# Kernel optimization log

Hardware: AMD Instinct MI355X
Metric: run time of the kernel (lower is better)

## Reference

```python
import jax, jax.numpy as jnp
import numpy as np

H = 4            # attention heads (HGTConv and SGFormer)
HID = 128        # hidden_dim
D = HID // H     # per-head dim in HGT
OUT = 128        # out_dim
L = 2            # number of HGT layers
NE, NA = 60000, 30000
E_EE, E_EA, E_AE = 150000, 75000, 75000


def setup_inputs() -> dict:
    ks = iter(jax.random.split(jax.random.key(0), 64))

    def nrm(shape, s=0.05):
        return jax.random.normal(next(ks), shape, dtype=jnp.float32) * s

    return {
        "x_entity": nrm((NE, HID), 1.0),
        "x_attr": nrm((NA, HID), 1.0),
        "Wkqv_ent": nrm((L, HID, 3 * HID)), "bkqv_ent": jnp.zeros((L, 3 * HID), jnp.float32),
        "Wkqv_att": nrm((L, HID, 3 * HID)), "bkqv_att": jnp.zeros((L, 3 * HID), jnp.float32),
        "Wout_ent": nrm((L, HID, HID)), "bout_ent": jnp.zeros((L, HID), jnp.float32),
        "Wout_att": nrm((L, HID, HID)), "bout_att": jnp.zeros((L, HID), jnp.float32),
        "skip_ent": jnp.ones((L,), jnp.float32), "skip_att": jnp.ones((L,), jnp.float32),
        "a_rel": nrm((L, 3, H, D, D), 0.1), "m_rel": nrm((L, 3, H, D, D), 0.1),
        "p_rel": jnp.ones((L, 3, H), jnp.float32),
        "ln_ent_g": jnp.ones((HID,), jnp.float32), "ln_ent_b": jnp.zeros((HID,), jnp.float32),
        "sg_fc_W": nrm((HID, HID)), "sg_fc_b": jnp.zeros((HID,), jnp.float32),
        "sg_ln0_g": jnp.ones((HID,), jnp.float32), "sg_ln0_b": jnp.zeros((HID,), jnp.float32),
        "sg_Wq": nrm((HID, HID * H)), "sg_bq": jnp.zeros((HID * H,), jnp.float32),
        "sg_Wk": nrm((HID, HID * H)), "sg_bk": jnp.zeros((HID * H,), jnp.float32),
        "sg_Wv": nrm((HID, HID * H)), "sg_bv": jnp.zeros((HID * H,), jnp.float32),
        "sg_ln1_g": jnp.ones((HID,), jnp.float32), "sg_ln1_b": jnp.zeros((HID,), jnp.float32),
        "proj_W1": nrm((HID, OUT)), "proj_b1": jnp.zeros((OUT,), jnp.float32),
        "proj_W2": nrm((OUT, OUT)), "proj_b2": jnp.zeros((OUT,), jnp.float32),
        "ei_ee": jax.random.randint(next(ks), (2, E_EE), 0, NE),
        "ei_ea": jnp.stack([jax.random.randint(next(ks), (E_EA,), 0, NE),
                            jax.random.randint(next(ks), (E_EA,), 0, NA)]),
        "ei_ae": jnp.stack([jax.random.randint(next(ks), (E_AE,), 0, NA),
                            jax.random.randint(next(ks), (E_AE,), 0, NE)]),
    }


def _ln(x, g, b, eps=1e-5):
    mu = x.mean(-1, keepdims=True)
    var = ((x - mu) ** 2).mean(-1, keepdims=True)
    return (x - mu) * jax.lax.rsqrt(var + eps) * g + b


def _seg_softmax(alpha, idx, n):
    # numerically stable softmax over edges grouped by destination node
    m = jax.ops.segment_max(alpha, idx, num_segments=n)
    e = jnp.exp(alpha - m[idx])
    s = jax.ops.segment_sum(e, idx, num_segments=n)
    return e / (s[idx] + 1e-16)


def _hgt_layer(x_e, x_a, Wkqv_e, bkqv_e, Wkqv_a, bkqv_a, Wout_e, bout_e,
               Wout_a, bout_a, sk_e, sk_a, a_rel, m_rel, p_rel,
               ei_ee, ei_ea, ei_ae):
    ne, na = x_e.shape[0], x_a.shape[0]
    # HeteroDictLinear producing [k|q|v], split along channels then reshape [N,H,D]
    kqv_e = (x_e @ Wkqv_e + bkqv_e).reshape(ne, 3, H, D)
    kqv_a = (x_a @ Wkqv_a + bkqv_a).reshape(na, 3, H, D)
    kd = {"e": kqv_e[:, 0], "a": kqv_a[:, 0]}
    qd = {"e": kqv_e[:, 1], "a": kqv_a[:, 1]}
    vd = {"e": kqv_e[:, 2], "a": kqv_a[:, 2]}
    nd = {"e": ne, "a": na}
    scale = 1.0 / float(np.sqrt(D))
    buf = {"e": [], "a": []}
    for t, (src, dst, ei) in enumerate([("e", "e", ei_ee), ("e", "a", ei_ea), ("a", "e", ei_ae)]):
        kt = jnp.einsum('nhd,hde->nhe', kd[src], a_rel[t])  # per-relation key transform (k_rel)
        vt = jnp.einsum('nhd,hde->nhe', vd[src], m_rel[t])  # per-relation value transform (v_rel)
        al = (qd[dst][ei[1]] * kt[ei[0]]).sum(-1) * p_rel[t] * scale  # [E,H]
        buf[dst].append((al, vt[ei[0]], ei[1]))
    outs = {}
    for dst in ("e", "a"):
        # joint softmax over ALL incoming edge types of this node type
        al = jnp.concatenate([b[0] for b in buf[dst]], 0)
        ve = jnp.concatenate([b[1] for b in buf[dst]], 0)
        ix = jnp.concatenate([b[2] for b in buf[dst]], 0)
        w = _seg_softmax(al, ix, nd[dst])
        outs[dst] = jax.ops.segment_sum(ve * w[..., None], ix,
                                        num_segments=nd[dst]).reshape(nd[dst], HID)
    o_e = jax.nn.gelu(outs["e"], approximate=False) @ Wout_e + bout_e
    o_a = jax.nn.gelu(outs["a"], approximate=False) @ Wout_a + bout_a
    g_e, g_a = jax.nn.sigmoid(sk_e), jax.nn.sigmoid(sk_a)
    return g_e * o_e + (1.0 - g_e) * x_e, g_a * o_a + (1.0 - g_a) * x_a


def reference(x_entity, x_attr, Wkqv_ent, bkqv_ent, Wkqv_att, bkqv_att,
              Wout_ent, bout_ent, Wout_att, bout_att, skip_ent, skip_att,
              a_rel, m_rel, p_rel, ln_ent_g, ln_ent_b,
              sg_fc_W, sg_fc_b, sg_ln0_g, sg_ln0_b, sg_Wq, sg_bq, sg_Wk, sg_bk,
              sg_Wv, sg_bv, sg_ln1_g, sg_ln1_b,
              proj_W1, proj_b1, proj_W2, proj_b2, ei_ee, ei_ea, ei_ae):
    h_e, h_a = x_entity, x_attr
    for l in range(L):
        h_e, h_a = _hgt_layer(h_e, h_a, Wkqv_ent[l], bkqv_ent[l], Wkqv_att[l], bkqv_att[l],
                              Wout_ent[l], bout_ent[l], Wout_att[l], bout_att[l],
                              skip_ent[l], skip_att[l], a_rel[l], m_rel[l], p_rel[l],
                              ei_ee, ei_ea, ei_ae)
        h_e = jax.nn.gelu(h_e, approximate=False)
        h_a = jax.nn.gelu(h_a, approximate=False)
    # SGFormer trans_conv: fc -> LN -> ReLU -> linear global attention -> residual -> LN
    n = h_e.shape[0]
    z0 = jax.nn.relu(_ln(h_e @ sg_fc_W + sg_fc_b, sg_ln0_g, sg_ln0_b))
    q = (z0 @ sg_Wq + sg_bq).reshape(n, H, HID)
    k = (z0 @ sg_Wk + sg_bk).reshape(n, H, HID)
    v = (z0 @ sg_Wv + sg_bv).reshape(n, H, HID)
    qs = q / jnp.linalg.norm(q)  # global Frobenius norm, as in SGFormer
    kn = k / jnp.linalg.norm(k)
    kvs = jnp.einsum('lhm,lhd->hmd', kn, v)
    num = jnp.einsum('nhm,hmd->nhd', qs, kvs) + float(n) * v
    den = jnp.einsum('nhm,hm->nh', qs, kn.sum(0))[..., None] + float(n)
    attn = (num / den).mean(1)  # mean over heads -> [n, HID]
    h_global = _ln(0.5 * attn + 0.5 * z0, sg_ln1_g, sg_ln1_b)  # residual alpha=0.5
    # alpha-blend (self.alpha = 0.1) + entity LayerNorm + projector MLP
    h_ent = _ln(0.9 * h_e + 0.1 * h_global, ln_ent_g, ln_ent_b)
    return jax.nn.relu(h_ent @ proj_W1 + proj_b1) @ proj_W2 + proj_b2
```

## Files before the change

kernel.cpp:

```cpp
#include <hip/hip_runtime.h>

#define NE 60000
#define NA 30000
#define E_EE 150000
#define E_EA 75000
#define E_AE 75000
#define SCALE 0.17677669529663689f

__device__ __forceinline__ float bf2f(unsigned short u) {
  return __uint_as_float(((unsigned)u) << 16);
}
__device__ __forceinline__ unsigned short f2bf(float f) {
  unsigned u = __float_as_uint(f);
  u = u + 0x7FFFu + ((u >> 16) & 1u);
  return (unsigned short)(u >> 16);
}
__device__ __forceinline__ float ldc(const float* p) { return *p; }
__device__ __forceinline__ float ldc(const unsigned short* p) { return bf2f(*p); }
__device__ __forceinline__ float gelu_f(float x) {
  return 0.5f * x * (1.0f + erff(x * 0.7071067811865476f));
}

__global__ __launch_bounds__(256) void wrel_k(
    const float* __restrict__ Wk_e, const float* __restrict__ Wk_a,
    const float* __restrict__ bk_e, const float* __restrict__ bk_a,
    const float* __restrict__ a_rel, const float* __restrict__ m_rel,
    float* __restrict__ Wkt, float* __restrict__ Wvt,
    float* __restrict__ bkt, float* __restrict__ bvt) {
  int t = blockIdx.x;
  int part = blockIdx.y;
  const float* W = (t < 2) ? Wk_e : Wk_a;
  const float* bb = (t < 2) ? bk_e : bk_a;
  const float* A = (part ? m_rel : a_rel) + t * 4096;
  int coff = part ? 256 : 0;
  float* Wo = (part ? Wvt : Wkt) + t * 16384;
  float* bo = (part ? bvt : bkt) + t * 128;
  __shared__ float As[4096];
  for (int u = threadIdx.x; u < 4096; u += 256) As[u] = A[u];
  __syncthreads();
  for (int u = threadIdx.x; u < 16384; u += 256) {
    int i = u >> 7, c = u & 127;
    int hh = c >> 5, e = c & 31;
    const float* wr = W + i * 384 + coff + hh * 32;
    const float* ar = As + hh * 1024 + e;
    float acc = 0.f;
#pragma unroll
    for (int d = 0; d < 32; ++d) acc = fmaf(wr[d], ar[d * 32], acc);
    Wo[u] = acc;
  }
  if (threadIdx.x < 128) {
    int c = threadIdx.x, hh = c >> 5, e = c & 31;
    const float* br = bb + coff + hh * 32;
    const float* ar = As + hh * 1024 + e;
    float acc = 0.f;
#pragma unroll
    for (int d = 0; d < 32; ++d) acc = fmaf(br[d], ar[d * 32], acc);
    bo[c] = acc;
  }
}

template <int ACT, int EPI>
__global__ __launch_bounds__(256) void gemm128_k(
    const float* __restrict__ X, int ldx,
    const float* __restrict__ W, int ldw,
    const float* __restrict__ bias, int N,
    float* __restrict__ fout, unsigned short* __restrict__ bout, int ldo,
    const float* __restrict__ skipp, float* __restrict__ ssq) {
  __shared__ float Xs[128 * 32];
  __shared__ float Ws[32 * 128];
  const int tid = threadIdx.x;
  const int ti = tid >> 4;
  const int tj = tid & 15;
  const int row0 = blockIdx.x * 128;
  const int cb = blockIdx.y * 128;
  const int c0 = cb + tj * 4;
  const int c1 = cb + 64 + tj * 4;

  float acc[8][8];
  {
    float bc[8] = {0.f, 0.f, 0.f, 0.f, 0.f, 0.f, 0.f, 0.f};
    if (bias) {
#pragma unroll
      for (int j = 0; j < 4; ++j) { bc[j] = bias[c0 + j]; bc[4 + j] = bias[c1 + j]; }
    }
#pragma unroll
    for (int i = 0; i < 8; ++i)
#pragma unroll
      for (int j = 0; j < 8; ++j) acc[i][j] = bc[j];
  }

  for (int ks = 0; ks < 128; ks += 32) {
    __syncthreads();
    for (int v = tid; v < 1024; v += 256) {
      int kq = v & 7, r = v >> 3;
      int rg = row0 + r; if (rg >= N) rg = N - 1;
      float4 x4 = *reinterpret_cast<const float4*>(X + (size_t)rg * ldx + ks + kq * 4);
      if (ACT == 1) {
        x4.x = gelu_f(x4.x); x4.y = gelu_f(x4.y);
        x4.z = gelu_f(x4.z); x4.w = gelu_f(x4.w);
      }
      *reinterpret_cast<float4*>(&Xs[r * 32 + ((kq ^ ((r >> 3) & 7)) << 2)]) = x4;
    }
    for (int v = tid; v < 1024; v += 256) {
      int cq = v & 31, k = v >> 5;
      *reinterpret_cast<float4*>(&Ws[k * 128 + cq * 4]) =
          *reinterpret_cast<const float4*>(W + (size_t)(ks + k) * ldw + cb + cq * 4);
    }
    __syncthreads();
#pragma unroll
    for (int k = 0; k < 32; k += 4) {
      float xr[8][4];
#pragma unroll
      for (int i = 0; i < 8; ++i)
        *reinterpret_cast<float4*>(xr[i]) = *reinterpret_cast<const float4*>(
            &Xs[(ti * 8 + i) * 32 + ((((k >> 2)) ^ (ti & 7)) << 2)]);
      float wr[4][8];
#pragma unroll
      for (int dk = 0; dk < 4; ++dk) {
        *reinterpret_cast<float4*>(&wr[dk][0]) =
            *reinterpret_cast<const float4*>(&Ws[(k + dk) * 128 + tj * 4]);
        *reinterpret_cast<float4*>(&wr[dk][4]) =
            *reinterpret_cast<const float4*>(&Ws[(k + dk) * 128 + 64 + tj * 4]);
      }
#pragma unroll
      for (int i = 0; i < 8; ++i)
#pragma unroll
        for (int dk = 0; dk < 4; ++dk)
#pragma unroll
          for (int j = 0; j < 8; ++j)
            acc[i][j] = fmaf(xr[i][dk], wr[dk][j], acc[i][j]);
    }
  }

  if (EPI == 0 || EPI == 1) {
#pragma unroll
    for (int i = 0; i < 8; ++i) {
      int rg = row0 + ti * 8 + i;
      if (rg < N) {
        float4 a = make_float4(acc[i][0], acc[i][1], acc[i][2], acc[i][3]);
        float4 b = make_float4(acc[i][4], acc[i][5], acc[i][6], acc[i][7]);
        if (EPI == 1) {
          a.x = fmaxf(a.x, 0.f); a.y = fmaxf(a.y, 0.f);
          a.z = fmaxf(a.z, 0.f); a.w = fmaxf(a.w, 0.f);
          b.x = fmaxf(b.x, 0.f); b.y = fmaxf(b.y, 0.f);
          b.z = fmaxf(b.z, 0.f); b.w = fmaxf(b.w, 0.f);
        }
        *reinterpret_cast<float4*>(fout + (size_t)rg * ldo + c0) = a;
        *reinterpret_cast<float4*>(fout + (size_t)rg * ldo + c1) = b;
      }
    }
  } else if (EPI == 2) {
    float loc = 0.f;
#pragma unroll
    for (int i = 0; i < 8; ++i) {
      int rg = row0 + ti * 8 + i;
      if (rg < N) {
        ushort4 s0, s1;
        s0.x = f2bf(acc[i][0]); s0.y = f2bf(acc[i][1]);
        s0.z = f2bf(acc[i][2]); s0.w = f2bf(acc[i][3]);
        s1.x = f2bf(acc[i][4]); s1.y = f2bf(acc[i][5]);
        s1.z = f2bf(acc[i][6]); s1.w = f2bf(acc[i][7]);
        *reinterpret_cast<ushort4*>(bout + (size_t)rg * ldo + c0) = s0;
        *reinterpret_cast<ushort4*>(bout + (size_t)rg * ldo + c1) = s1;
#pragma unroll
        for (int j = 0; j < 8; ++j) loc += acc[i][j] * acc[i][j];
      }
    }
    if (ssq) {
      __syncthreads();
      Xs[tid] = loc;
      __syncthreads();
      if (tid < 128) Xs[tid] += Xs[tid + 128];
      __syncthreads();
      if (tid < 64) {
        float v = Xs[tid] + Xs[tid + 64];
#pragma unroll
        for (int m = 32; m > 0; m >>= 1) v += __shfl_down(v, m, 64);
        if (tid == 0) atomicAdd(ssq, v);
      }
    }
  } else {
    float g = 1.f / (1.f + expf(-*skipp));
    float g1 = 1.f - g;
#pragma unroll
    for (int i = 0; i < 8; ++i) {
      int rg = row0 + ti * 8 + i;
      if (rg < N) {
        float4 o0 = *reinterpret_cast<const float4*>(fout + (size_t)rg * ldo + c0);
        float4 o1 = *reinterpret_cast<const float4*>(fout + (size_t)rg * ldo + c1);
        float4 a, b;
        a.x = gelu_f(g * acc[i][0] + g1 * o0.x);
        a.y = gelu_f(g * acc[i][1] + g1 * o0.y);
        a.z = gelu_f(g * acc[i][2] + g1 * o0.z);
        a.w = gelu_f(g * acc[i][3] + g1 * o0.w);
        b.x = gelu_f(g * acc[i][4] + g1 * o1.x);
        b.y = gelu_f(g * acc[i][5] + g1 * o1.y);
        b.z = gelu_f(g * acc[i][6] + g1 * o1.z);
        b.w = gelu_f(g * acc[i][7] + g1 * o1.w);
        *reinterpret_cast<float4*>(fout + (size_t)rg * ldo + c0) = a;
        *reinterpret_cast<float4*>(fout + (size_t)rg * ldo + c1) = b;
      }
    }
  }
}

__global__ __launch_bounds__(256) void deg_k(const int* __restrict__ ei, int E,
                                             int* __restrict__ deg) {
  int i = blockIdx.x * 256 + threadIdx.x;
  if (i < E) atomicAdd(&deg[ei[E + i]], 1);
}

__global__ __launch_bounds__(1024) void scan_k(int* __restrict__ deg_cursor,
                                               int* __restrict__ rowptr, int n) {
  __shared__ int sd[1024];
  __shared__ int carry;
  int tid = threadIdx.x;
  if (tid == 0) carry = 0;
  __syncthreads();
  for (int base = 0; base < n; base += 1024) {
    int v = (base + tid < n) ? deg_cursor[base + tid] : 0;
    sd[tid] = v;
    __syncthreads();
    for (int off = 1; off < 1024; off <<= 1) {
      int t = (tid >= off) ? sd[tid - off] : 0;
      __syncthreads();
      sd[tid] += t;
      __syncthreads();
    }
    int c0 = carry;
    if (base + tid < n) {
      int excl = c0 + sd[tid] - v;
      rowptr[base + tid] = excl;
      deg_cursor[base + tid] = excl;
    }
    __syncthreads();
    if (tid == 0) carry = c0 + sd[1023];
    __syncthreads();
  }
  if (tid == 0) rowptr[n] = carry;
}

__global__ __launch_bounds__(256) void fill_k(const int* __restrict__ ei, int E,
                                              int* __restrict__ cursor,
                                              int* __restrict__ entries,
                                              int srcoff, int tag) {
  int i = blockIdx.x * 256 + threadIdx.x;
  if (i < E) {
    int pos = atomicAdd(&cursor[ei[E + i]], 1);
    entries[pos] = (ei[i] + srcoff) | (tag << 30);
  }
}

__global__ __launch_bounds__(256) void hgt_gather_k(
    const float* __restrict__ q, const unsigned short* __restrict__ ktbl,
    const unsigned short* __restrict__ vtbl, const int* __restrict__ rowptr,
    const int* __restrict__ entries, const float* __restrict__ pbase, int nd,
    float* __restrict__ out) {
  int g = blockIdx.x * 8 + (threadIdx.x >> 5);
  int dst = g >> 2, h = g & 3, c = threadIdx.x & 31;
  if (dst >= nd) return;
  int col = h * 32 + c;
  float qv = q[(size_t)dst * 128 + col];
  int i0 = rowptr[dst], i1 = rowptr[dst + 1];
  float sum = 0.f, acc = 0.f;
  for (int i = i0; i < i1; ++i) {
    int e = entries[i];
    int lin = e & 0x3FFFFFFF;
    int tag = (unsigned)e >> 30;
    float part = qv * bf2f(ktbl[(size_t)lin * 128 + col]);
#pragma unroll
    for (int m = 16; m > 0; m >>= 1) part += __shfl_xor(part, m);
    float w = expf(part * SCALE * pbase[tag * 8 + h]);
    sum += w;
    acc = fmaf(w, bf2f(vtbl[(size_t)lin * 128 + col]), acc);
  }
  out[(size_t)dst * 128 + col] = acc / (sum + 1e-16f);
}

template <typename AT, typename BT>
__global__ __launch_bounds__(128) void ln_k(const AT* __restrict__ A,
                                            const BT* __restrict__ B, float alpha,
                                            float beta, const float* __restrict__ g,
                                            const float* __restrict__ b,
                                            float* __restrict__ out, int relu) {
  int row = blockIdx.x;
  int t = threadIdx.x;
  float v = alpha * ldc(A + (size_t)row * 128 + t);
  if (B) v += beta * ldc(B + (size_t)row * 128 + t);
  float s1 = v, s2 = v * v;
#pragma unroll
  for (int m = 32; m > 0; m >>= 1) {
    s1 += __shfl_xor(s1, m, 64);
    s2 += __shfl_xor(s2, m, 64);
  }
  __shared__ float r1[2], r2[2];
  int w = t >> 6;
  if ((t & 63) == 0) { r1[w] = s1; r2[w] = s2; }
  __syncthreads();
  float S1 = r1[0] + r1[1], S2 = r2[0] + r2[1];
  float mu = S1 * (1.f / 128.f);
  float var = S2 * (1.f / 128.f) - mu * mu;
  float rr = rsqrtf(fmaxf(var, 0.f) + 1e-5f);
  float o = (v - mu) * rr * g[t] + b[t];
  if (relu) o = fmaxf(o, 0.f);
  out[(size_t)row * 128 + t] = o;
}

__global__ __launch_bounds__(256) void kvsred_k(const unsigned short* __restrict__ Kb,
                                                const unsigned short* __restrict__ Vb,
                                                float* __restrict__ part,
                                                float* __restrict__ ksum, int chunk) {
  const int h = blockIdx.y;
  const int n0 = blockIdx.x * chunk;
  const int iters = chunk >> 3;
  __shared__ float ks[8][132];
  __shared__ float vs[8][132];
  const int tid = threadIdx.x;
  const int ti = tid >> 4, tj = tid & 15;

  const int sw = tid >> 7;
  const int sni = (tid >> 4) & 7;
  const int sc = (tid & 15) << 3;
  const unsigned short* src =
      (sw ? Vb : Kb) + (size_t)(n0 + sni) * 512 + h * 128 + sc;
  float* dstrow = (sw ? &vs[0][0] : &ks[0][0]) + sni * 132 + sc;

  float acc[8][8];
#pragma unroll
  for (int i = 0; i < 8; ++i)
#pragma unroll
    for (int j = 0; j < 8; ++j) acc[i][j] = 0.f;
  float ksloc = 0.f;

  uint4 r = *reinterpret_cast<const uint4*>(src);
  for (int it = 0; it < iters; ++it) {
    __syncthreads();
    float4 lo, hi;
    lo.x = bf2f((unsigned short)(r.x & 0xffffu)); lo.y = bf2f((unsigned short)(r.x >> 16));
    lo.z = bf2f((unsigned short)(r.y & 0xffffu)); lo.w = bf2f((unsigned short)(r.y >> 16));
    hi.x = bf2f((unsigned short)(r.z & 0xffffu)); hi.y = bf2f((unsigned short)(r.z >> 16));
    hi.z = bf2f((unsigned short)(r.w & 0xffffu)); hi.w = bf2f((unsigned short)(r.w >> 16));
    *reinterpret_cast<float4*>(dstrow) = lo;
    *reinterpret_cast<float4*>(dstrow + 4) = hi;
    if (it + 1 < iters)
      r = *reinterpret_cast<const uint4*>(src + (size_t)(it + 1) * 8 * 512);
    __syncthreads();
#pragma unroll
    for (int ni = 0; ni < 8; ++ni) {
      float kk[8], vv[8];
      *reinterpret_cast<float4*>(kk) =
          *reinterpret_cast<const float4*>(&ks[ni][ti * 4]);
      *reinterpret_cast<float4*>(kk + 4) =
          *reinterpret_cast<const float4*>(&ks[ni][64 + ti * 4]);
      *reinterpret_cast<float4*>(vv) =
          *reinterpret_cast<const float4*>(&vs[ni][tj * 4]);
      *reinterpret_cast<float4*>(vv + 4) =
          *reinterpret_cast<const float4*>(&vs[ni][64 + tj * 4]);
#pragma unroll
      for (int i = 0; i < 8; ++i)
#pragma unroll
        for (int j = 0; j < 8; ++j) acc[i][j] = fmaf(kk[i], vv[j], acc[i][j]);
      if (tid < 128) ksloc += ks[ni][tid];
    }
  }
  float* pb = part + (size_t)(blockIdx.x * 4 + h) * 16384;
#pragma unroll
  for (int i = 0; i < 8; ++i) {
    int m = ti * 4 + (i & 3) + ((i >> 2) << 6);
    *reinterpret_cast<float4*>(pb + m * 128 + tj * 4) =
        make_float4(acc[i][0], acc[i][1], acc[i][2], acc[i][3]);
    *reinterpret_cast<float4*>(pb + m * 128 + 64 + tj * 4) =
        make_float4(acc[i][4], acc[i][5], acc[i][6], acc[i][7]);
  }
  if (tid < 128) atomicAdd(&ksum[h * 128 + tid], ksloc);
}

__global__ __launch_bounds__(256) void kvsfin_k(const float* __restrict__ part,
                                                float* __restrict__ kvs, int G) {
  int c = blockIdx.x * 256 + threadIdx.x;
  int hh = c >> 14, md = c & 16383;
  const float* p = part + (size_t)hh * 16384 + md;
  float s = 0.f;
#pragma unroll 4
  for (int g = 0; g < G; ++g) s += p[(size_t)g * 65536];
  kvs[c] = s;
}

__global__ __launch_bounds__(256) void sgapply_k(const unsigned short* __restrict__ Qb,
                                                 const unsigned short* __restrict__ Vb,
                                                 const float* __restrict__ kvs,
                                                 const float* __restrict__ ksum,
                                                 const float* __restrict__ ssqq,
                                                 const float* __restrict__ ssqk,
                                                 unsigned short* __restrict__ attnb) {
  __shared__ float Qs[32 * 132];
  __shared__ float Ws[64 * 128];
  __shared__ float dred[32][9];
  __shared__ float den_s[32];
  __shared__ float fsh;
  const int tid = threadIdx.x;
  const int ct = tid & 31, rt = tid >> 5;
  const int row0 = blockIdx.x * 32;
  if (tid == 0) fsh = 1.0f / (sqrtf(*ssqq) * sqrtf(*ssqk));
  float out[4][4];
#pragma unroll
  for (int i = 0; i < 4; ++i)
#pragma unroll
    for (int j = 0; j < 4; ++j) out[i][j] = 0.f;

  for (int h = 0; h < 4; ++h) {
    __syncthreads();
    for (int u = tid; u < 1024; u += 256) {
      int r = u >> 5, c = (u & 31) << 2;
      ushort4 q4 = *reinterpret_cast<const ushort4*>(
          Qb + (size_t)(row0 + r) * 512 + h * 128 + c);
      float4 v = make_float4(bf2f(q4.x), bf2f(q4.y), bf2f(q4.z), bf2f(q4.w));
      *reinterpret_cast<float4*>(&Qs[r * 132 + c]) = v;
    }
    __syncthreads();
    {
      int r = tid >> 3, seg = tid & 7;
      const float* kp = ksum + h * 128 + seg * 16;
      const float* qp = Qs + r * 132 + seg * 16;
      float p = 0.f;
#pragma unroll
      for (int c = 0; c < 16; ++c) p = fmaf(qp[c], kp[c], p);
      dred[r][seg] = p;
    }
    __syncthreads();
    if (tid < 32) {
      float t = 0.f;
#pragma unroll
      for (int s8 = 0; s8 < 8; ++s8) t += dred[tid][s8];
      den_s[tid] = t * fsh + 60000.0f;
    }
    float acc[4][4];
#pragma unroll
    for (int i = 0; i < 4; ++i)
#pragma unroll
      for (int j = 0; j < 4; ++j) acc[i][j] = 0.f;
    for (int kk = 0; kk < 2; ++kk) {
      __syncthreads();
      for (int u = tid; u < 2048; u += 256) {
        int r = u >> 5, c = (u & 31) << 2;
        *reinterpret_cast<float4*>(&Ws[r * 128 + c]) =
            *reinterpret_cast<const float4*>(kvs + (size_t)h * 16384 +
                                             (size_t)(kk * 64 + r) * 128 + c);
      }
      __syncthreads();
#pragma unroll 4
      for (int k = 0; k < 64; k += 4) {
        float w[4][4];
#pragma unroll
        for (int dk = 0; dk < 4; ++dk)
          *reinterpret_cast<float4*>(w[dk]) =
              *reinterpret_cast<const float4*>(&Ws[(k + dk) * 128 + (ct << 2)]);
#pragma unroll
        for (int i = 0; i < 4; ++i) {
          float xv[4];
          *reinterpret_cast<float4*>(xv) =
              *reinterpret_cast<const float4*>(&Qs[(rt * 4 + i) * 132 + kk * 64 + k]);
#pragma unroll
          for (int dk = 0; dk < 4; ++dk)
#pragma unroll
            for (int j = 0; j < 4; ++j) acc[i][j] = fmaf(xv[dk], w[dk][j], acc[i][j]);
        }
      }
    }
    float f = fsh;
#pragma unroll
    for (int i = 0; i < 4; ++i) {
      int rg = row0 + rt * 4 + i;
      ushort4 v4 = *reinterpret_cast<const ushort4*>(
          Vb + (size_t)rg * 512 + h * 128 + (ct << 2));
      float rd = 1.0f / den_s[rt * 4 + i];
      out[i][0] += (acc[i][0] * f + 60000.0f * bf2f(v4.x)) * rd;
      out[i][1] += (acc[i][1] * f + 60000.0f * bf2f(v4.y)) * rd;
      out[i][2] += (acc[i][2] * f + 60000.0f * bf2f(v4.z)) * rd;
      out[i][3] += (acc[i][3] * f + 60000.0f * bf2f(v4.w)) * rd;
    }
  }
#pragma unroll
  for (int i = 0; i < 4; ++i) {
    int rg = row0 + rt * 4 + i;
    ushort4 s4;
    s4.x = f2bf(0.25f * out[i][0]); s4.y = f2bf(0.25f * out[i][1]);
    s4.z = f2bf(0.25f * out[i][2]); s4.w = f2bf(0.25f * out[i][3]);
    *reinterpret_cast<ushort4*>(attnb + (size_t)rg * 128 + (ct << 2)) = s4;
  }
}

extern "C" void kernel_launch(void* const* d_in, const int* in_sizes, int n_in,
                              void* d_out, int out_size, void* d_ws, size_t ws_size,
                              hipStream_t stream) {
  const float* x_ent = (const float*)d_in[0];
  const float* x_att = (const float*)d_in[1];
  const float* Wkqv_e = (const float*)d_in[2];
  const float* bkqv_e = (const float*)d_in[3];
  const float* Wkqv_a = (const float*)d_in[4];
  const float* bkqv_a = (const float*)d_in[5];
  const float* Wout_e = (const float*)d_in[6];
  const float* bout_e = (const float*)d_in[7];
  const float* Wout_a = (const float*)d_in[8];
  const float* bout_a = (const float*)d_in[9];
  const float* skip_e = (const float*)d_in[10];
  const float* skip_a = (const float*)d_in[11];
  const float* a_rel = (const float*)d_in[12];
  const float* m_rel = (const float*)d_in[13];
  const float* p_rel = (const float*)d_in[14];
  const float* ln_ent_g = (const float*)d_in[15];
  const float* ln_ent_b = (const float*)d_in[16];
  const float* sg_fc_W = (const float*)d_in[17];
  const float* sg_fc_b = (const float*)d_in[18];
  const float* sg_ln0_g = (const float*)d_in[19];
  const float* sg_ln0_b = (const float*)d_in[20];
  const float* sg_Wq = (const float*)d_in[21];
  const float* sg_bq = (const float*)d_in[22];
  const float* sg_Wk = (const float*)d_in[23];
  const float* sg_bk = (const float*)d_in[24];
  const float* sg_Wv = (const float*)d_in[25];
  const float* sg_bv = (const float*)d_in[26];
  const float* sg_ln1_g = (const float*)d_in[27];
  const float* sg_ln1_b = (const float*)d_in[28];
  const float* proj_W1 = (const float*)d_in[29];
  const float* proj_b1 = (const float*)d_in[30];
  const float* proj_W2 = (const float*)d_in[31];
  const float* proj_b2 = (const float*)d_in[32];
  const int* ei_ee = (const int*)d_in[33];
  const int* ei_ea = (const int*)d_in[34];
  const int* ei_ae = (const int*)d_in[35];

  char* ws = (char*)d_ws;
  const size_t O_HE = 0;
  const size_t O_HA = 30720000;
  const size_t O_Z0 = 46080000;
  const size_t O_WKT = 76800000;
  const size_t O_WVT = 76996608;
  const size_t O_BKT = 77193216;
  const size_t O_BVT = 77194752;
  const size_t O_KVS = 77196288;
  const size_t O_RPE = 77460544;
  const size_t O_RPA = O_RPE + 240064;
  const size_t O_CUE = O_RPA + 120064;
  const size_t O_CUA = O_CUE + 240000;
  const size_t O_ENE = O_CUA + 120000;
  const size_t O_ENA = O_ENE + 900000;
  const size_t O_UN = O_ENA + 300000;
  float* q_e = (float*)(ws + O_UN);
  float* q_a = (float*)(ws + O_UN + 30720000);
  unsigned short* ktbl = (unsigned short*)(ws + O_UN + 46080000);
  unsigned short* vtbl = (unsigned short*)(ws + O_UN + 84480000);
  float* tmpf = (float*)(ws + O_UN);
  unsigned short* Vb = (unsigned short*)(ws + O_UN);
  unsigned short* KQb = (unsigned short*)(ws + O_UN + 61440000);
  unsigned short* attnb = (unsigned short*)(ws + O_HA);

  float* h_e = (float*)(ws + O_HE);
  float* h_a = (float*)(ws + O_HA);
  float* z0 = (float*)(ws + O_Z0);
  float* Wkt = (float*)(ws + O_WKT);
  float* Wvt = (float*)(ws + O_WVT);
  float* bkt = (float*)(ws + O_BKT);
  float* bvt = (float*)(ws + O_BVT);
  float* kvs = (float*)(ws + O_KVS);
  float* ksum = (float*)(ws + O_KVS + 262144);
  float* ssq_q = (float*)(ws + O_KVS + 262144 + 2048);
  float* ssq_k = ssq_q + 1;
  int* rowptr_e = (int*)(ws + O_RPE);
  int* rowptr_a = (int*)(ws + O_RPA);
  int* cursor_e = (int*)(ws + O_CUE);
  int* cursor_a = (int*)(ws + O_CUA);
  int* entries_e = (int*)(ws + O_ENE);
  int* entries_a = (int*)(ws + O_ENA);

  const int GB_E = (NE + 127) / 128;
  const int GB_A = (NA + 127) / 128;

  hipMemcpyAsync(h_e, x_ent, (size_t)NE * 128 * 4, hipMemcpyDeviceToDevice, stream);
  hipMemcpyAsync(h_a, x_att, (size_t)NA * 128 * 4, hipMemcpyDeviceToDevice, stream);

  hipMemsetAsync(ws + O_CUE, 0, 360000, stream);
  deg_k<<<(E_EE + 255) / 256, 256, 0, stream>>>(ei_ee, E_EE, cursor_e);
  deg_k<<<(E_AE + 255) / 256, 256, 0, stream>>>(ei_ae, E_AE, cursor_e);
  deg_k<<<(E_EA + 255) / 256, 256, 0, stream>>>(ei_ea, E_EA, cursor_a);
  scan_k<<<1, 1024, 0, stream>>>(cursor_e, rowptr_e, NE);
  scan_k<<<1, 1024, 0, stream>>>(cursor_a, rowptr_a, NA);
  fill_k<<<(E_EE + 255) / 256, 256, 0, stream>>>(ei_ee, E_EE, cursor_e, entries_e, 0, 0);
  fill_k<<<(E_AE + 255) / 256, 256, 0, stream>>>(ei_ae, E_AE, cursor_e, entries_e, NE, 1);
  fill_k<<<(E_EA + 255) / 256, 256, 0, stream>>>(ei_ea, E_EA, cursor_a, entries_a, 0, 0);

  for (int l = 0; l < 2; ++l) {
    const float* Wke = Wkqv_e + (size_t)l * 49152;
    const float* Wka = Wkqv_a + (size_t)l * 49152;
    const float* bke = bkqv_e + (size_t)l * 384;
    const float* bka = bkqv_a + (size_t)l * 384;

    wrel_k<<<dim3(3, 2), 256, 0, stream>>>(Wke, Wka, bke, bka,
                                           a_rel + (size_t)l * 12288,
                                           m_rel + (size_t)l * 12288, Wkt, Wvt, bkt, bvt);
    gemm128_k<0, 0><<<GB_E, 256, 0, stream>>>(h_e, 128, Wke + 128, 384, bke + 128, NE,
                                              q_e, nullptr, 128, nullptr, nullptr);
    gemm128_k<0, 0><<<GB_A, 256, 0, stream>>>(h_a, 128, Wka + 128, 384, bka + 128, NA,
                                              q_a, nullptr, 128, nullptr, nullptr);
    gemm128_k<0, 2><<<GB_E, 256, 0, stream>>>(h_e, 128, Wkt, 128, bkt, NE,
                                              nullptr, ktbl, 128, nullptr, nullptr);
    gemm128_k<0, 2><<<GB_A, 256, 0, stream>>>(h_a, 128, Wkt + 2 * 16384, 128,
                                              bkt + 2 * 128, NA, nullptr,
                                              ktbl + (size_t)NE * 128, 128, nullptr, nullptr);
    gemm128_k<0, 2><<<GB_E, 256, 0, stream>>>(h_e, 128, Wkt + 1 * 16384, 128,
                                              bkt + 1 * 128, NE, nullptr,
                                              ktbl + (size_t)90000 * 128, 128, nullptr, nullptr);
    gemm128_k<0, 2><<<GB_E, 256, 0, stream>>>(h_e, 128, Wvt, 128, bvt, NE,
                                              nullptr, vtbl, 128, nullptr, nullptr);
    gemm128_k<0, 2><<<GB_A, 256, 0, stream>>>(h_a, 128, Wvt + 2 * 16384, 128,
                                              bvt + 2 * 128, NA, nullptr,
                                              vtbl + (size_t)NE * 128, 128, nullptr, nullptr);
    gemm128_k<0, 2><<<GB_E, 256, 0, stream>>>(h_e, 128, Wvt + 1 * 16384, 128,
                                              bvt + 1 * 128, NE, nullptr,
                                              vtbl + (size_t)90000 * 128, 128, nullptr, nullptr);
    hgt_gather_k<<<30000, 256, 0, stream>>>(q_e, ktbl, vtbl, rowptr_e, entries_e,
                                            p_rel + (size_t)l * 12, NE, q_e);
    hgt_gather_k<<<15000, 256, 0, stream>>>(q_a, ktbl + (size_t)90000 * 128,
                                            vtbl + (size_t)90000 * 128, rowptr_a,
                                            entries_a, p_rel + (size_t)l * 12 + 4, NA, q_a);
    gemm128_k<1, 3><<<GB_E, 256, 0, stream>>>(q_e, 128, Wout_e + (size_t)l * 16384, 128,
                                              bout_e + (size_t)l * 128, NE, h_e, nullptr,
                                              128, skip_e + l, nullptr);
    gemm128_k<1, 3><<<GB_A, 256, 0, stream>>>(q_a, 128, Wout_a + (size_t)l * 16384, 128,
                                              bout_a + (size_t)l * 128, NA, h_a, nullptr,
                                              128, skip_a + l, nullptr);
  }

  gemm128_k<0, 0><<<GB_E, 256, 0, stream>>>(h_e, 128, sg_fc_W, 128, sg_fc_b, NE,
                                            tmpf, nullptr, 128, nullptr, nullptr);
  ln_k<float, float><<<NE, 128, 0, stream>>>(tmpf, nullptr, 1.f, 0.f, sg_ln0_g,
                                             sg_ln0_b, z0, 1);
  hipMemsetAsync(ws + O_KVS, 0, 264256, stream);
  gemm128_k<0, 2><<<dim3(GB_E, 4), 256, 0, stream>>>(z0, 128, sg_Wv, 512, sg_bv, NE,
                                                     nullptr, Vb, 512, nullptr, nullptr);
  gemm128_k<0, 2><<<dim3(GB_E, 4), 256, 0, stream>>>(z0, 128, sg_Wk, 512, sg_bk, NE,
                                                     nullptr, KQb, 512, nullptr, ssq_k);
  kvsred_k<<<dim3(100, 4), 256, 0, stream>>>(KQb, Vb, (float*)d_out, ksum, 600);
  kvsfin_k<<<256, 256, 0, stream>>>((const float*)d_out, kvs, 100);
  gemm128_k<0, 2><<<dim3(GB_E, 4), 256, 0, stream>>>(z0, 128, sg_Wq, 512, sg_bq, NE,
                                                     nullptr, KQb, 512, nullptr, ssq_q);
  sgapply_k<<<NE / 32, 256, 0, stream>>>(KQb, Vb, kvs, ksum, ssq_q, ssq_k, attnb);
  ln_k<unsigned short, float><<<NE, 128, 0, stream>>>(attnb, z0, 0.5f, 0.5f, sg_ln1_g,
                                                      sg_ln1_b, z0, 0);
  ln_k<float, float><<<NE, 128, 0, stream>>>(h_e, z0, 0.9f, 0.1f, ln_ent_g, ln_ent_b,
                                             h_e, 0);
  gemm128_k<0, 1><<<GB_E, 256, 0, stream>>>(h_e, 128, proj_W1, 128, proj_b1, NE,
                                            z0, nullptr, 128, nullptr, nullptr);
  gemm128_k<0, 0><<<GB_E, 256, 0, stream>>>(z0, 128, proj_W2, 128, proj_b2, NE,
                                            (float*)d_out, nullptr, 128, nullptr, nullptr);
}
```

Measured before the change: 2.038 ms.

## Retile SGFormer apply kernel to 128-row blocks with 8x8 register tiles

Rewrites sgapply_k so each block handles 128 rows with 8x8 per-thread output tiles instead of 32 rows with 4x4 tiles. The K dimension is streamed in chunks of 32 through a swizzled shared-memory layout. The denominator dot product with ksum is folded into the main FMA loop, which removes the separate reduction pass and its extra barriers. The goal is more arithmetic reuse per shared-memory load and each kvs tile loaded by fewer blocks. The cost is higher register pressure and lower occupancy, plus bounds clamping for a partial last block.

```diff
diff --git a/kernel.cpp b/kernel.cpp
--- a/kernel.cpp
+++ b/kernel.cpp
@@ -392,101 +392,110 @@
                                                  const float* __restrict__ ksum,
                                                  const float* __restrict__ ssqq,
                                                  const float* __restrict__ ssqk,
-                                                 unsigned short* __restrict__ attnb) {
-  __shared__ float Qs[32 * 132];
-  __shared__ float Ws[64 * 128];
-  __shared__ float dred[32][9];
-  __shared__ float den_s[32];
-  __shared__ float fsh;
+                                                 unsigned short* __restrict__ attnb,
+                                                 int N) {
+  __shared__ float Xs[128 * 32];
+  __shared__ float Ws[32 * 128];
+  __shared__ float kss[32];
+  __shared__ float fsh_s;
   const int tid = threadIdx.x;
-  const int ct = tid & 31, rt = tid >> 5;
-  const int row0 = blockIdx.x * 32;
-  if (tid == 0) fsh = 1.0f / (sqrtf(*ssqq) * sqrtf(*ssqk));
-  float out[4][4];
-#pragma unroll
-  for (int i = 0; i < 4; ++i)
-#pragma unroll
-    for (int j = 0; j < 4; ++j) out[i][j] = 0.f;
+  const int ti = tid >> 4;
+  const int tj = tid & 15;
+  const int row0 = blockIdx.x * 128;
+  if (tid == 0) fsh_s = 1.0f / (sqrtf(*ssqq) * sqrtf(*ssqk));
+
+  float out[8][8];
+#pragma unroll
+  for (int i = 0; i < 8; ++i)
+#pragma unroll
+    for (int j = 0; j < 8; ++j) out[i][j] = 0.f;
 
   for (int h = 0; h < 4; ++h) {
-    __syncthreads();
-    for (int u = tid; u < 1024; u += 256) {
-      int r = u >> 5, c = (u & 31) << 2;
-      ushort4 q4 = *reinterpret_cast<const ushort4*>(
-          Qb + (size_t)(row0 + r) * 512 + h * 128 + c);
-      float4 v = make_float4(bf2f(q4.x), bf2f(q4.y), bf2f(q4.z), bf2f(q4.w));
-      *reinterpret_cast<float4*>(&Qs[r * 132 + c]) = v;
-    }
-    __syncthreads();
-    {
-      int r = tid >> 3, seg = tid & 7;
-      const float* kp = ksum + h * 128 + seg * 16;
-      const float* qp = Qs + r * 132 + seg * 16;
-      float p = 0.f;
-#pragma unroll
-      for (int c = 0; c < 16; ++c) p = fmaf(qp[c], kp[c], p);
-      dred[r][seg] = p;
-    }
-    __syncthreads();
-    if (tid < 32) {
-      float t = 0.f;
-#pragma unroll
-      for (int s8 = 0; s8 < 8; ++s8) t += dred[tid][s8];
-      den_s[tid] = t * fsh + 60000.0f;
-    }
-    float acc[4][4];
-#pragma unroll
-    for (int i = 0; i < 4; ++i)
-#pragma unroll
-      for (int j = 0; j < 4; ++j) acc[i][j] = 0.f;
-    for (int kk = 0; kk < 2; ++kk) {
+    float acc[8][8];
+    float den[8];
+#pragma unroll
+    for (int i = 0; i < 8; ++i) {
+      den[i] = 0.f;
+#pragma unroll
+      for (int j = 0; j < 8; ++j) acc[i][j] = 0.f;
+    }
+    for (int ks = 0; ks < 128; ks += 32) {
       __syncthreads();
-      for (int u = tid; u < 2048; u += 256) {
-        int r = u >> 5, c = (u & 31) << 2;
-        *reinterpret_cast<float4*>(&Ws[r * 128 + c]) =
+      for (int v = tid; v < 1024; v += 256) {
+        int kq = v & 7, r = v >> 3;
+        int rg = row0 + r; if (rg >= N) rg = N - 1;
+        ushort4 q4 = *reinterpret_cast<const ushort4*>(
+            Qb + (size_t)rg * 512 + h * 128 + ks + kq * 4);
+        float4 x4 = make_float4(bf2f(q4.x), bf2f(q4.y), bf2f(q4.z), bf2f(q4.w));
+        *reinterpret_cast<float4*>(&Xs[r * 32 + ((kq ^ ((r >> 3) & 7)) << 2)]) = x4;
+      }
+      for (int v = tid; v < 1024; v += 256) {
+        int cq = v & 31, k = v >> 5;
+        *reinterpret_cast<float4*>(&Ws[k * 128 + cq * 4]) =
             *reinterpret_cast<const float4*>(kvs + (size_t)h * 16384 +
-                                             (size_t)(kk * 64 + r) * 128 + c);
-      }
+                                             (size_t)(ks + k) * 128 + cq * 4);
+      }
+      if (tid < 32) kss[tid] = ksum[h * 128 + ks + tid];
       __syncthreads();
-#pragma unroll 4
-      for (int k = 0; k < 64; k += 4) {
-        float w[4][4];
-#pragma unroll
-        for (int dk = 0; dk < 4; ++dk)
-          *reinterpret_cast<float4*>(w[dk]) =
-              *reinterpret_cast<const float4*>(&Ws[(k + dk) * 128 + (ct << 2)]);
-#pragma unroll
-        for (int i = 0; i < 4; ++i) {
-          float xv[4];
-          *reinterpret_cast<float4*>(xv) =
-              *reinterpret_cast<const float4*>(&Qs[(rt * 4 + i) * 132 + kk * 64 + k]);
-#pragma unroll
-          for (int dk = 0; dk < 4; ++dk)
-#pragma unroll
-            for (int j = 0; j < 4; ++j) acc[i][j] = fmaf(xv[dk], w[dk][j], acc[i][j]);
+#pragma unroll
+      for (int k = 0; k < 32; k += 4) {
+        float xr[8][4];
+#pragma unroll
+        for (int i = 0; i < 8; ++i)
+          *reinterpret_cast<float4*>(xr[i]) = *reinterpret_cast<const float4*>(
+              &Xs[(ti * 8 + i) * 32 + ((((k >> 2)) ^ (ti & 7)) << 2)]);
+        float wr[4][8];
+        float kv[4];
+#pragma unroll
+        for (int dk = 0; dk < 4; ++dk) {
+          *reinterpret_cast<float4*>(&wr[dk][0]) =
+              *reinterpret_cast<const float4*>(&Ws[(k + dk) * 128 + tj * 4]);
+          *reinterpret_cast<float4*>(&wr[dk][4]) =
+              *reinterpret_cast<const float4*>(&Ws[(k + dk) * 128 + 64 + tj * 4]);
+          kv[dk] = kss[k + dk];
         }
-      }
-    }
-    float f = fsh;
-#pragma unroll
-    for (int i = 0; i < 4; ++i) {
-      int rg = row0 + rt * 4 + i;
-      ushort4 v4 = *reinterpret_cast<const ushort4*>(
-          Vb + (size_t)rg * 512 + h * 128 + (ct << 2));
-      float rd = 1.0f / den_s[rt * 4 + i];
-      out[i][0] += (acc[i][0] * f + 60000.0f * bf2f(v4.x)) * rd;
-      out[i][1] += (acc[i][1] * f + 60000.0f * bf2f(v4.y)) * rd;
-      out[i][2] += (acc[i][2] * f + 60000.0f * bf2f(v4.z)) * rd;
-      out[i][3] += (acc[i][3] * f + 60000.0f * bf2f(v4.w)) * rd;
-    }
-  }
-#pragma unroll
-  for (int i = 0; i < 4; ++i) {
-    int rg = row0 + rt * 4 + i;
-    ushort4 s4;
-    s4.x = f2bf(0.25f * out[i][0]); s4.y = f2bf(0.25f * out[i][1]);
-    s4.z = f2bf(0.25f * out[i][2]); s4.w = f2bf(0.25f * out[i][3]);
-    *reinterpret_cast<ushort4*>(attnb + (size_t)rg * 128 + (ct << 2)) = s4;
+#pragma unroll
+        for (int i = 0; i < 8; ++i)
+#pragma unroll
+          for (int dk = 0; dk < 4; ++dk) {
+            den[i] = fmaf(xr[i][dk], kv[dk], den[i]);
+#pragma unroll
+            for (int j = 0; j < 8; ++j)
+              acc[i][j] = fmaf(xr[i][dk], wr[dk][j], acc[i][j]);
+          }
+      }
+    }
+    float f = fsh_s;
+#pragma unroll
+    for (int i = 0; i < 8; ++i) {
+      int rg = row0 + ti * 8 + i; if (rg >= N) rg = N - 1;
+      ushort4 v0 = *reinterpret_cast<const ushort4*>(
+          Vb + (size_t)rg * 512 + h * 128 + tj * 4);
+      ushort4 v1 = *reinterpret_cast<const ushort4*>(
+          Vb + (size_t)rg * 512 + h * 128 + 64 + tj * 4);
+      float rd = 1.0f / (den[i] * f + 60000.0f);
+      out[i][0] += (acc[i][0] * f + 60000.0f * bf2f(v0.x)) * rd;
+      out[i][1] += (acc[i][1] * f + 60000.0f * bf2f(v0.y)) * rd;
+      out[i][2] += (acc[i][2] * f + 60000.0f * bf2f(v0.z)) * rd;
+      out[i][3] += (acc[i][3] * f + 60000.0f * bf2f(v0.w)) * rd;
+      out[i][4] += (acc[i][4] * f + 60000.0f * bf2f(v1.x)) * rd;
+      out[i][5] += (acc[i][5] * f + 60000.0f * bf2f(v1.y)) * rd;
+      out[i][6] += (acc[i][6] * f + 60000.0f * bf2f(v1.z)) * rd;
+      out[i][7] += (acc[i][7] * f + 60000.0f * bf2f(v1.w)) * rd;
+    }
+  }
+#pragma unroll
+  for (int i = 0; i < 8; ++i) {
+    int rg = row0 + ti * 8 + i;
+    if (rg < N) {
+      ushort4 s0, s1;
+      s0.x = f2bf(0.25f * out[i][0]); s0.y = f2bf(0.25f * out[i][1]);
+      s0.z = f2bf(0.25f * out[i][2]); s0.w = f2bf(0.25f * out[i][3]);
+      s1.x = f2bf(0.25f * out[i][4]); s1.y = f2bf(0.25f * out[i][5]);
+      s1.z = f2bf(0.25f * out[i][6]); s1.w = f2bf(0.25f * out[i][7]);
+      *reinterpret_cast<ushort4*>(attnb + (size_t)rg * 128 + tj * 4) = s0;
+      *reinterpret_cast<ushort4*>(attnb + (size_t)rg * 128 + 64 + tj * 4) = s1;
+    }
   }
 }
 
@@ -644,7 +653,7 @@
   kvsfin_k<<<256, 256, 0, stream>>>((const float*)d_out, kvs, 100);
   gemm128_k<0, 2><<<dim3(GB_E, 4), 256, 0, stream>>>(z0, 128, sg_Wq, 512, sg_bq, NE,
                                                      nullptr, KQb, 512, nullptr, ssq_q);
-  sgapply_k<<<NE / 32, 256, 0, stream>>>(KQb, Vb, kvs, ksum, ssq_q, ssq_k, attnb);
+  sgapply_k<<<GB_E, 256, 0, stream>>>(KQb, Vb, kvs, ksum, ssq_q, ssq_k, attnb, NE);
   ln_k<unsigned short, float><<<NE, 128, 0, stream>>>(attnb, z0, 0.5f, 0.5f, sg_ln1_g,
                                                       sg_ln1_b, z0, 0);
   ln_k<float, float><<<NE, 128, 0, stream>>>(h_e, z0, 0.9f, 0.1f, ln_ent_g, ln_ent_b,
```

New measurement: 2.135 ms. 4.7% more time.
